# Performance work log

Measured on AMD Instinct MI355X. Metric: run time of the kernel, lower is better.

Reference implementation:

```python
import jax, jax.numpy as jnp
import numpy as np

HW = 24       # image_size // patch_size
HEAD = 16     # vision num_attention_heads
B, T, C, H = 8, 8, 1024, 4096


def _sincos_1d(d, pos):
    omega = np.arange(d // 2, dtype=np.float32) / (d / 2.0)
    omega = 1.0 / 10000 ** omega
    out = np.einsum('m,d->md', pos.reshape(-1).astype(np.float32), omega)
    return np.concatenate([np.sin(out), np.cos(out)], axis=1)


def _pos_embed_3d(embed_dim, grid_size, t_size):
    ds = embed_dim // 4 * 3
    dt = embed_dim // 4
    gh = np.arange(grid_size, dtype=np.float32)
    grid = np.stack(np.meshgrid(gh, gh), axis=0).reshape(2, -1)  # (w, h) order as in source
    spatial = np.concatenate([_sincos_1d(ds // 2, grid[0]), _sincos_1d(ds // 2, grid[1])], axis=1)  # [g*g, ds]
    temporal = _sincos_1d(dt, np.arange(t_size, dtype=np.float32))  # [t, dt]
    spatial = np.repeat(spatial[np.newaxis], t_size, axis=0)                 # [t, g*g, ds]
    temporal = np.repeat(temporal[:, np.newaxis], grid_size ** 2, axis=1)    # [t, g*g, dt]
    emb = np.concatenate([temporal, spatial], axis=-1)
    return emb.reshape(1, t_size * grid_size ** 2, embed_dim).astype(np.float32)


def setup_inputs() -> dict:
    key = jax.random.key(0)
    k1, k2, k3 = jax.random.split(key, 3)
    x = jax.random.normal(k1, (B, T * HW * HW, C), dtype=jnp.float32)
    W1 = jax.random.normal(k2, (C, H), dtype=jnp.float32) * 0.02
    b1 = jnp.zeros((H,), jnp.float32)
    W2 = jax.random.normal(k3, (H, H), dtype=jnp.float32) * 0.02
    b2 = jnp.zeros((H,), jnp.float32)
    pos_embed = jnp.asarray(_pos_embed_3d(C, HW, T))
    return {"x": x, "pos_embed": pos_embed, "W1": W1, "b1": b1, "W2": W2, "b2": b2,
            "local_num_frames": T}


def _merge(x, unm_idx, src_idx, dst_idx):
    # ToMe merge: gather unmatched src tokens, scatter-add matched src into dst.
    src, dst = x[:, ::2], x[:, 1::2]
    unm = jnp.take_along_axis(src, unm_idx[:, :, None], axis=1)   # [b, t1-r, c]
    sel = jnp.take_along_axis(src, src_idx[:, :, None], axis=1)   # [b, r, c]
    dst = jax.vmap(lambda d, i, s: d.at[i].add(s))(dst, dst_idx, sel)
    return jnp.concatenate([unm, dst], axis=1)


def _merge_tokens(x, target, head):
    b, p, c = x.shape
    # static merge schedule (same logic as torch merge_tokens)
    rs, tmp = [], p
    while tmp != target:
        if tmp - target <= tmp // 2:
            rs.append(tmp - target)
            break
        rs.append(tmp // 2)
        tmp -= tmp // 2
    dim = c // head
    size = jnp.ones((b, p, 1), x.dtype)
    for r in rs:
        bb, pp, _ = x.shape
        # metric/index computation is under no_grad in the original
        metric = jax.lax.stop_gradient(x).reshape(bb, pp, head, dim).mean(2)
        metric = metric / jnp.linalg.norm(metric, axis=-1, keepdims=True)
        a_m, b_m = metric[:, ::2], metric[:, 1::2]
        scores = jnp.einsum('bic,bjc->bij', a_m, b_m)  # [b, ta, tb]
        node_max = scores.max(-1)
        node_idx = scores.argmax(-1)
        edge_idx = jnp.argsort(-node_max, axis=-1)      # descending
        unm_idx, src_idx = edge_idx[:, r:], edge_idx[:, :r]
        dst_idx = jnp.take_along_axis(node_idx, src_idx, axis=1)
        # weighted-average merge (merge_wavg)
        x = _merge(x * size, unm_idx, src_idx, dst_idx)
        size = _merge(size, unm_idx, src_idx, dst_idx)
        x = x / size
    return x


def reference(x, pos_embed, W1, b1, W2, b2, local_num_frames):
    x = x + pos_embed.astype(x.dtype)
    x = _merge_tokens(x, local_num_frames * 16, HEAD)
    h = jax.nn.gelu(x @ W1 + b1, approximate=False)  # nn.GELU() is exact erf gelu
    return h @ W2 + b2
```

## Files before the change

### kernel.cpp

```cpp
#include <hip/hip_runtime.h>
#include <hip/hip_bf16.h>
#include <math.h>
#include <stdint.h>

typedef unsigned short u16;
typedef __attribute__((ext_vector_type(8))) short short8;
typedef __attribute__((ext_vector_type(4))) float floatx4;

#define NB 8
#define P0 4608
#define C0 1024
#define H0 4096

__global__ void detect_mode_kernel(const uint32_t* __restrict__ pe_words, int* __restrict__ mode) {
  *mode = (pe_words[64] != 0u) ? 1 : 0;
}

__device__ __forceinline__ float load_in(const void* p, size_t idx, int mode) {
  if (mode) return __bfloat162float(((const __hip_bfloat16*)p)[idx]);
  return ((const float*)p)[idx];
}

__device__ __forceinline__ float4 load4(const void* p, size_t idx, int mode) {
  float4 r;
  if (mode) {
    ushort4 u = *(const ushort4*)((const u16*)p + idx);
    r.x = __bfloat162float(*(__hip_bfloat16*)&u.x);
    r.y = __bfloat162float(*(__hip_bfloat16*)&u.y);
    r.z = __bfloat162float(*(__hip_bfloat16*)&u.z);
    r.w = __bfloat162float(*(__hip_bfloat16*)&u.w);
  } else {
    r = *(const float4*)((const float*)p + idx);
  }
  return r;
}

__device__ __forceinline__ void write_hilo(u16* __restrict__ m2, size_t tok, int lane, float v) {
  __hip_bfloat16 hi = __float2bfloat16(v);
  float hif = __bfloat162float(hi);
  __hip_bfloat16 lo = __float2bfloat16(v - hif);
  m2[tok * 128 + lane] = *(u16*)&hi;
  m2[tok * 128 + 64 + lane] = *(u16*)&lo;
}

__global__ void metric_in_kernel(const void* __restrict__ x, const void* __restrict__ pos,
                                 const int* __restrict__ mode, u16* __restrict__ m2) {
  int tok = blockIdx.x * 4 + (threadIdx.x >> 6);
  int lane = threadIdx.x & 63;
  if (tok >= NB * P0) return;
  int b = tok / P0, t = tok - b * P0;
  int md = *mode;
  size_t xbase = ((size_t)b * P0 + t) * C0 + lane;
  size_t pbase = (size_t)t * C0 + lane;
  float s = 0.f;
#pragma unroll
  for (int h = 0; h < 16; ++h)
    s += load_in(x, xbase + h * 64, md) + load_in(pos, pbase + h * 64, md);
  s *= (1.f / 16.f);
  float sq = s * s;
#pragma unroll
  for (int off = 1; off < 64; off <<= 1) sq += __shfl_xor(sq, off, 64);
  write_hilo(m2, (size_t)tok, lane, s / sqrtf(sq));
}

__global__ void metric_f32_kernel(const float* __restrict__ x, u16* __restrict__ m2, int p) {
  int tok = blockIdx.x * 4 + (threadIdx.x >> 6);
  int lane = threadIdx.x & 63;
  if (tok >= NB * p) return;
  const float* xr = x + (size_t)tok * C0 + lane;
  float s = 0.f;
#pragma unroll
  for (int h = 0; h < 16; ++h) s += xr[h * 64];
  s *= (1.f / 16.f);
  float sq = s * s;
#pragma unroll
  for (int off = 1; off < 64; off <<= 1) sq += __shfl_xor(sq, off, 64);
  write_hilo(m2, (size_t)tok, lane, s / sqrtf(sq));
}

__global__ __launch_bounds__(256) void score_mfma_kernel(const u16* __restrict__ M2,
                                                         int p, int p2, int jT2,
                                                         float* __restrict__ pm,
                                                         int* __restrict__ pi) {
  const int bi = blockIdx.x, ii = blockIdx.y, b = blockIdx.z;
  const int t = threadIdx.x, w = t >> 6, L = t & 63;
  const int wr = w >> 1, wc = w & 1;
  const int fr = L & 15, fo = (L >> 4) * 8;
  const u16* Mb = M2 + (size_t)b * p * 128;

  floatx4 acc[4][4];
#pragma unroll
  for (int mt = 0; mt < 4; ++mt)
#pragma unroll
    for (int nt = 0; nt < 4; ++nt) acc[mt][nt] = (floatx4){0.f, 0.f, 0.f, 0.f};

  const u16* arp[4];
  const u16* brp[4];
#pragma unroll
  for (int mt = 0; mt < 4; ++mt) {
    int i = ii * 128 + wr * 64 + mt * 16 + fr;
    int ta = 2 * i;
    if (ta > p - 2) ta = p - 2;
    arp[mt] = Mb + (size_t)ta * 128 + fo;
    int j = bi * 128 + wc * 64 + mt * 16 + fr;
    int tb = 2 * j + 1;
    if (tb > p - 1) tb = p - 1;
    brp[mt] = Mb + (size_t)tb * 128 + fo;
  }

#pragma unroll
  for (int ks = 0; ks < 2; ++ks) {
    short8 ah[4], al[4], bh[4], bl[4];
#pragma unroll
    for (int mt = 0; mt < 4; ++mt) {
      ah[mt] = *(const short8*)(arp[mt] + ks * 32);
      al[mt] = *(const short8*)(arp[mt] + ks * 32 + 64);
      bh[mt] = *(const short8*)(brp[mt] + ks * 32);
      bl[mt] = *(const short8*)(brp[mt] + ks * 32 + 64);
    }
#pragma unroll
    for (int mt = 0; mt < 4; ++mt)
#pragma unroll
      for (int nt = 0; nt < 4; ++nt) {
        acc[mt][nt] = __builtin_amdgcn_mfma_f32_16x16x32_bf16(ah[mt], bh[nt], acc[mt][nt], 0, 0, 0);
        acc[mt][nt] = __builtin_amdgcn_mfma_f32_16x16x32_bf16(ah[mt], bl[nt], acc[mt][nt], 0, 0, 0);
        acc[mt][nt] = __builtin_amdgcn_mfma_f32_16x16x32_bf16(al[mt], bh[nt], acc[mt][nt], 0, 0, 0);
        acc[mt][nt] = __builtin_amdgcn_mfma_f32_16x16x32_bf16(al[mt], bl[nt], acc[mt][nt], 0, 0, 0);
      }
  }

  const int gi4 = (L >> 4) * 4;
#pragma unroll
  for (int mt = 0; mt < 4; ++mt) {
#pragma unroll
    for (int reg = 0; reg < 4; ++reg) {
      int i = ii * 128 + wr * 64 + mt * 16 + gi4 + reg;
      float bm = -INFINITY;
      int bj = 0x7fffffff;
#pragma unroll
      for (int nt = 0; nt < 4; ++nt) {
        int j = bi * 128 + wc * 64 + nt * 16 + fr;
        float v = acc[mt][nt][reg];
        if (j < p2 && v > bm) { bm = v; bj = j; }
      }
#pragma unroll
      for (int mk = 1; mk < 16; mk <<= 1) {
        float om = __shfl_xor(bm, mk, 64);
        int oj = __shfl_xor(bj, mk, 64);
        if (om > bm || (om == bm && oj < bj)) { bm = om; bj = oj; }
      }
      if (fr == 0 && i < p2) {
        size_t o = ((size_t)b * 2304 + i) * jT2 + bi * 2 + wc;
        pm[o] = bm;
        pi[o] = bj;
      }
    }
  }
}

__global__ void argmax_combine_kernel(const float* __restrict__ pm, const int* __restrict__ pi,
                                      int p2, int jT, float* __restrict__ nmax,
                                      int* __restrict__ nidx, int* __restrict__ head,
                                      int* __restrict__ nxt) {
  int g = blockIdx.x * 256 + threadIdx.x;
  if (g >= NB * p2) return;
  int b = g / p2, i = g - b * p2;
  const float* r = pm + ((size_t)b * 2304 + i) * jT;
  const int* ri = pi + ((size_t)b * 2304 + i) * jT;
  float best = r[0];
  int bidx = ri[0];
  for (int k = 1; k < jT; ++k) {
    if (r[k] > best || (r[k] == best && ri[k] < bidx)) { best = r[k]; bidx = ri[k]; }
  }
  nmax[g] = best;
  nidx[g] = bidx;
  int d = bidx;
  if ((unsigned)d >= (unsigned)p2) d = 0;
  nxt[g] = atomicExch(&head[(size_t)b * p2 + d], i);
}

__global__ void init_heads_kernel(int* __restrict__ h, int n) {
  int g = blockIdx.x * 256 + threadIdx.x;
  if (g < n) h[g] = -1;
}

__global__ __launch_bounds__(256) void merge_gather_in(const void* __restrict__ x,
                                                       const void* __restrict__ pos,
                                                       const int* __restrict__ mode,
                                                       const int* __restrict__ head,
                                                       const int* __restrict__ nxt,
                                                       float* __restrict__ xo,
                                                       float* __restrict__ so, int p2) {
  int tj = blockIdx.x;
  int b = tj / p2, j = tj - b * p2;
  int c = threadIdx.x * 4;
  int md = *mode;
  __shared__ int sl[64];
  __shared__ int s_n, s_cur;
  size_t xb = ((size_t)b * P0 + 2 * j + 1) * C0 + c;
  size_t pb = (size_t)(2 * j + 1) * C0 + c;
  float4 xa = load4(x, xb, md), pa = load4(pos, pb, md);
  float4 acc = {xa.x + pa.x, xa.y + pa.y, xa.z + pa.z, xa.w + pa.w};
  float cnt = 1.f;
  if (threadIdx.x == 0) s_cur = head[tj];
  __syncthreads();
  int cur = s_cur;
  while (cur != -1) {
    if (threadIdx.x == 0) {
      int n = 0, cc = cur;
      while (cc != -1 && n < 64) {
        sl[n++] = cc;
        cc = nxt[(size_t)b * p2 + cc];
      }
      s_n = n;
      s_cur = cc;
    }
    __syncthreads();
    int n = s_n;
    cur = s_cur;
    for (int k = 0; k < n; ++k) {
      int i = sl[k];
      size_t exb = ((size_t)b * P0 + 2 * i) * C0 + c;
      size_t epb = (size_t)(2 * i) * C0 + c;
      float4 ea = load4(x, exb, md), ep = load4(pos, epb, md);
      acc.x += ea.x + ep.x;
      acc.y += ea.y + ep.y;
      acc.z += ea.z + ep.z;
      acc.w += ea.w + ep.w;
      cnt += 1.f;
    }
    __syncthreads();
  }
  float inv = 1.f / cnt;
  float4 o = {acc.x * inv, acc.y * inv, acc.z * inv, acc.w * inv};
  *(float4*)(xo + (size_t)tj * C0 + c) = o;
  if (threadIdx.x == 0) so[tj] = cnt;
}

__global__ __launch_bounds__(256) void merge_gather_f(const float* __restrict__ xi,
                                                      const float* __restrict__ si,
                                                      const int* __restrict__ head,
                                                      const int* __restrict__ nxt,
                                                      float* __restrict__ xo,
                                                      float* __restrict__ so, int p, int p2) {
  int tj = blockIdx.x;
  int b = tj / p2, j = tj - b * p2;
  int c = threadIdx.x * 4;
  __shared__ int sl[64];
  __shared__ int s_n, s_cur;
  float sz = si[(size_t)b * p + 2 * j + 1];
  float4 v = *(const float4*)(xi + ((size_t)b * p + 2 * j + 1) * C0 + c);
  float4 acc = {v.x * sz, v.y * sz, v.z * sz, v.w * sz};
  float ssum = sz;
  if (threadIdx.x == 0) s_cur = head[tj];
  __syncthreads();
  int cur = s_cur;
  while (cur != -1) {
    if (threadIdx.x == 0) {
      int n = 0, cc = cur;
      while (cc != -1 && n < 64) {
        sl[n++] = cc;
        cc = nxt[(size_t)b * p2 + cc];
      }
      s_n = n;
      s_cur = cc;
    }
    __syncthreads();
    int n = s_n;
    cur = s_cur;
    for (int k = 0; k < n; ++k) {
      int i = sl[k];
      float szi = si[(size_t)b * p + 2 * i];
      float4 e = *(const float4*)(xi + ((size_t)b * p + 2 * i) * C0 + c);
      acc.x += e.x * szi;
      acc.y += e.y * szi;
      acc.z += e.z * szi;
      acc.w += e.w * szi;
      ssum += szi;
    }
    __syncthreads();
  }
  float inv = 1.f / ssum;
  float4 o = {acc.x * inv, acc.y * inv, acc.z * inv, acc.w * inv};
  *(float4*)(xo + (size_t)tj * C0 + c) = o;
  if (threadIdx.x == 0) so[tj] = ssum;
}

__global__ void rank_kernel(const float* __restrict__ nmax, const int* __restrict__ nidx,
                            int* __restrict__ unm_map, int* __restrict__ src_ord,
                            int* __restrict__ src_dst) {
  int b = blockIdx.x;
  int i = threadIdx.x;
  __shared__ float v[72];
  __shared__ int nx[72];
  if (i < 72) { v[i] = nmax[b * 72 + i]; nx[i] = nidx[b * 72 + i]; }
  __syncthreads();
  if (i < 72) {
    float vi = v[i];
    int rank = 0;
    for (int k = 0; k < 72; ++k) {
      float vk = v[k];
      rank += (vk > vi) || (vk == vi && k < i);
    }
    if (rank < 16) {
      int d = nx[i];
      if ((unsigned)d >= 72u) d = 0;
      src_ord[b * 16 + rank] = i;
      src_dst[b * 16 + rank] = d;
    } else {
      unm_map[b * 56 + (rank - 16)] = i;
    }
  }
}

__global__ void final_init(const float* __restrict__ x5, const float* __restrict__ s5,
                           const int* __restrict__ unm_map, float* __restrict__ xf,
                           float* __restrict__ sf) {
  int bt = blockIdx.x;
  int b = bt >> 7, tk = bt & 127;
  int c = threadIdx.x * 4;
  float4 o;
  float szo;
  if (tk < 56) {
    int se = unm_map[b * 56 + tk];
    if ((unsigned)se >= 72u) se = 0;
    o = *(const float4*)(x5 + ((size_t)b * 144 + 2 * se) * C0 + c);
    szo = 1.f;
  } else {
    int j = tk - 56;
    float sz = s5[b * 144 + 2 * j + 1];
    float4 v = *(const float4*)(x5 + ((size_t)b * 144 + 2 * j + 1) * C0 + c);
    o.x = v.x * sz; o.y = v.y * sz; o.z = v.z * sz; o.w = v.w * sz;
    szo = sz;
  }
  *(float4*)(xf + (size_t)bt * C0 + c) = o;
  if (threadIdx.x == 0) sf[bt] = szo;
}

__global__ void final_scatter(const float* __restrict__ x5, const float* __restrict__ s5,
                              const int* __restrict__ src_ord, const int* __restrict__ src_dst,
                              float* __restrict__ xf, float* __restrict__ sf) {
  int bk = blockIdx.x;
  int b = bk >> 4, k = bk & 15;
  int c = threadIdx.x * 4;
  int st = src_ord[b * 16 + k], dst = src_dst[b * 16 + k];
  if ((unsigned)st >= 72u) st = 0;
  if ((unsigned)dst >= 72u) dst = 0;
  float sz = s5[b * 144 + 2 * st];
  float4 v = *(const float4*)(x5 + ((size_t)b * 144 + 2 * st) * C0 + c);
  float* out = xf + ((size_t)(b * 128 + 56 + dst)) * C0 + c;
  atomicAdd(out + 0, v.x * sz);
  atomicAdd(out + 1, v.y * sz);
  atomicAdd(out + 2, v.z * sz);
  atomicAdd(out + 3, v.w * sz);
  if (threadIdx.x == 0) atomicAdd(sf + b * 128 + 56 + dst, sz);
}

__global__ void final_div_cvt(const float* __restrict__ xf, const float* __restrict__ sf,
                              __hip_bfloat16* __restrict__ xb) {
  int bt = blockIdx.x;
  int c = threadIdx.x * 4;
  float sz = sf[bt];
  float4 v = *(const float4*)(xf + (size_t)bt * C0 + c);
  __hip_bfloat16* o = xb + (size_t)bt * C0 + c;
  o[0] = __float2bfloat16(v.x / sz);
  o[1] = __float2bfloat16(v.y / sz);
  o[2] = __float2bfloat16(v.z / sz);
  o[3] = __float2bfloat16(v.w / sz);
}

__global__ void transpose_in(const void* __restrict__ in, const int* __restrict__ mode,
                             u16* __restrict__ out, int K, int N) {
  __shared__ u16 tile[64][65];
  int n0 = blockIdx.x * 64, k0 = blockIdx.y * 64;
  int t = threadIdx.x;
  int md = *mode;
  int r = t >> 4, c4 = (t & 15) * 4;
#pragma unroll
  for (int pass = 0; pass < 4; ++pass) {
    int row = r + pass * 16;
#pragma unroll
    for (int e = 0; e < 4; ++e) {
      float v = load_in(in, (size_t)(k0 + row) * N + n0 + c4 + e, md);
      __hip_bfloat16 bv = __float2bfloat16(v);
      tile[row][c4 + e] = *(u16*)&bv;
    }
  }
  __syncthreads();
#pragma unroll
  for (int pass = 0; pass < 4; ++pass) {
    int row = r + pass * 16;
    ushort4 o;
    o.x = tile[c4][row]; o.y = tile[c4 + 1][row]; o.z = tile[c4 + 2][row]; o.w = tile[c4 + 3][row];
    *(ushort4*)(out + (size_t)(n0 + row) * K + k0 + c4) = o;
  }
}

__global__ __launch_bounds__(256) void gemm_bt(const u16* __restrict__ A,
                                               const u16* __restrict__ BT,
                                               const void* __restrict__ bias,
                                               const int* __restrict__ mode,
                                               void* __restrict__ C, int M, int N,
                                               int K, int act, int out_sel) {
  __shared__ __align__(16) u16 As[128 * 64];
  __shared__ __align__(16) u16 Bs[128 * 64];
  const int t = threadIdx.x, w = t >> 6, L = t & 63;
  const int m0 = blockIdx.y * 128, n0 = blockIdx.x * 128;
  const int wr = w >> 1, wc = w & 1;
  const int md = *mode;
  floatx4 acc[4][4];
#pragma unroll
  for (int a = 0; a < 4; ++a)
#pragma unroll
    for (int bb = 0; bb < 4; ++bb) acc[a][bb] = (floatx4){0.f, 0.f, 0.f, 0.f};
  const int fr = L & 15, fq = (L >> 4) * 8;
  const int srow = t >> 3, sc8 = (t & 7) * 8;
  for (int k0 = 0; k0 < K; k0 += 64) {
#pragma unroll
    for (int q = 0; q < 4; ++q) {
      int row = srow + q * 32;
      *(short8*)(As + row * 64 + sc8) =
          *(const short8*)(A + (size_t)(m0 + row) * K + k0 + sc8);
      *(short8*)(Bs + row * 64 + sc8) =
          *(const short8*)(BT + (size_t)(n0 + row) * K + k0 + sc8);
    }
    __syncthreads();
#pragma unroll
    for (int kh = 0; kh < 2; ++kh) {
      short8 af[4], bfr[4];
#pragma unroll
      for (int mt = 0; mt < 4; ++mt)
        af[mt] = *(const short8*)(As + (wr * 64 + mt * 16 + fr) * 64 + kh * 32 + fq);
#pragma unroll
      for (int nt = 0; nt < 4; ++nt)
        bfr[nt] = *(const short8*)(Bs + (wc * 64 + nt * 16 + fr) * 64 + kh * 32 + fq);
#pragma unroll
      for (int mt = 0; mt < 4; ++mt)
#pragma unroll
        for (int nt = 0; nt < 4; ++nt)
          acc[mt][nt] =
              __builtin_amdgcn_mfma_f32_16x16x32_bf16(af[mt], bfr[nt], acc[mt][nt], 0, 0, 0);
    }
    __syncthreads();
  }
#pragma unroll
  for (int mt = 0; mt < 4; ++mt)
#pragma unroll
    for (int nt = 0; nt < 4; ++nt) {
      int n = n0 + wc * 64 + nt * 16 + fr;
      float bz = load_in(bias, n, md);
#pragma unroll
      for (int rr = 0; rr < 4; ++rr) {
        int m = m0 + wr * 64 + mt * 16 + (L >> 4) * 4 + rr;
        float v = acc[mt][nt][rr] + bz;
        if (act) v = 0.5f * v * (1.f + erff(v * 0.70710678118654752f));
        size_t idx = (size_t)m * N + n;
        if (out_sel == 0 || md) {
          __hip_bfloat16 bv = __float2bfloat16(v);
          ((u16*)C)[idx] = *(u16*)&bv;
        } else {
          ((float*)C)[idx] = v;
        }
      }
    }
}

extern "C" void kernel_launch(void* const* d_in, const int* in_sizes, int n_in, void* d_out,
                              int out_size, void* d_ws, size_t ws_size, hipStream_t stream) {
  const void* x = d_in[0];
  const void* pe = d_in[1];
  const void* W1 = d_in[2];
  const void* b1 = d_in[3];
  const void* W2 = d_in[4];
  const void* b2 = d_in[5];

  char* base = (char*)d_ws;
  size_t off = 0;
  auto alloc = [&](size_t bytes) -> void* {
    void* p = base + off;
    off += (bytes + 255) & ~(size_t)255;
    return p;
  };
  int* mode = (int*)alloc(256);
  u16* m2 = (u16*)alloc((size_t)NB * 4608 * 128 * 2);
  float* pm = (float*)alloc((size_t)NB * 2304 * 36 * 4);
  int* pi = (int*)alloc((size_t)NB * 2304 * 36 * 4);
  float* nmax = (float*)alloc((size_t)NB * 2304 * 4);
  int* nidx = (int*)alloc((size_t)NB * 2304 * 4);
  float* bufA = (float*)alloc((size_t)NB * 2304 * C0 * 4);
  float* bufB = (float*)alloc((size_t)NB * 1152 * C0 * 4);
  float* s1 = (float*)alloc((size_t)NB * 2304 * 4);
  float* s2 = (float*)alloc((size_t)NB * 1152 * 4);
  float* s3 = (float*)alloc((size_t)NB * 576 * 4);
  float* s4 = (float*)alloc((size_t)NB * 288 * 4);
  float* s5 = (float*)alloc((size_t)NB * 144 * 4);
  float* sf = (float*)alloc((size_t)NB * 128 * 4);
  int* unm_map = (int*)alloc((size_t)NB * 56 * 4);
  int* src_ord = (int*)alloc((size_t)NB * 16 * 4);
  int* src_dst = (int*)alloc((size_t)NB * 16 * 4);
  u16* xfb = (u16*)alloc((size_t)NB * 128 * C0 * 2);
  u16* hbuf = (u16*)alloc((size_t)1024 * H0 * 2);
  u16* w1t = (u16*)alloc((size_t)H0 * C0 * 2);
  u16* w2t = (u16*)alloc((size_t)H0 * H0 * 2);
  int* heads = (int*)alloc((size_t)NB * 4536 * 4);
  int* nxt = (int*)alloc((size_t)NB * 2304 * 4);
  if (off > ws_size) return;

  int* h_it[6];
  h_it[0] = heads;
  h_it[1] = h_it[0] + NB * 2304;
  h_it[2] = h_it[1] + NB * 1152;
  h_it[3] = h_it[2] + NB * 576;
  h_it[4] = h_it[3] + NB * 288;
  h_it[5] = h_it[4] + NB * 144;

  float* x1 = bufA;
  float* x2 = bufB;
  float* x3 = bufA;
  float* x4 = bufB;
  float* x5 = bufA;
  float* xf = bufB;

  detect_mode_kernel<<<1, 1, 0, stream>>>((const uint32_t*)pe, mode);
  init_heads_kernel<<<(NB * 4536 + 255) / 256, 256, 0, stream>>>(heads, NB * 4536);

  transpose_in<<<dim3(4096 / 64, 1024 / 64), 256, 0, stream>>>(W1, mode, w1t, 1024, 4096);
  transpose_in<<<dim3(4096 / 64, 4096 / 64), 256, 0, stream>>>(W2, mode, w2t, 4096, 4096);

  metric_in_kernel<<<NB * P0 / 4, 256, 0, stream>>>(x, pe, mode, m2);
  score_mfma_kernel<<<dim3(18, 18, NB), 256, 0, stream>>>(m2, 4608, 2304, 36, pm, pi);
  argmax_combine_kernel<<<(NB * 2304 + 255) / 256, 256, 0, stream>>>(pm, pi, 2304, 36, nmax,
                                                                     nidx, h_it[0], nxt);
  merge_gather_in<<<NB * 2304, 256, 0, stream>>>(x, pe, mode, h_it[0], nxt, x1, s1, 2304);

  float* xs_in[4] = {x1, x2, x3, x4};
  float* ss_in[4] = {s1, s2, s3, s4};
  float* xs_out[4] = {x2, x3, x4, x5};
  float* ss_out[4] = {s2, s3, s4, s5};
  int ps[5] = {2304, 1152, 576, 288, 144};
  for (int it = 0; it < 4; ++it) {
    int p = ps[it], p2 = ps[it + 1];
    int iT = (p2 + 127) / 128, jT = (p2 + 127) / 128;
    metric_f32_kernel<<<NB * p / 4, 256, 0, stream>>>(xs_in[it], m2, p);
    score_mfma_kernel<<<dim3(jT, iT, NB), 256, 0, stream>>>(m2, p, p2, 2 * jT, pm, pi);
    argmax_combine_kernel<<<(NB * p2 + 255) / 256, 256, 0, stream>>>(pm, pi, p2, 2 * jT, nmax,
                                                                     nidx, h_it[it + 1], nxt);
    merge_gather_f<<<NB * p2, 256, 0, stream>>>(xs_in[it], ss_in[it], h_it[it + 1], nxt,
                                                xs_out[it], ss_out[it], p, p2);
  }

  metric_f32_kernel<<<NB * 144 / 4, 256, 0, stream>>>(x5, m2, 144);
  score_mfma_kernel<<<dim3(1, 1, NB), 256, 0, stream>>>(m2, 144, 72, 2, pm, pi);
  argmax_combine_kernel<<<(NB * 72 + 255) / 256, 256, 0, stream>>>(pm, pi, 72, 2, nmax, nidx,
                                                                   h_it[5], nxt);
  rank_kernel<<<NB, 128, 0, stream>>>(nmax, nidx, unm_map, src_ord, src_dst);
  final_init<<<NB * 128, 256, 0, stream>>>(x5, s5, unm_map, xf, sf);
  final_scatter<<<NB * 16, 256, 0, stream>>>(x5, s5, src_ord, src_dst, xf, sf);
  final_div_cvt<<<NB * 128, 256, 0, stream>>>(xf, sf, (__hip_bfloat16*)xfb);

  gemm_bt<<<dim3(4096 / 128, 1024 / 128), 256, 0, stream>>>(xfb, w1t, b1, mode, hbuf, 1024, 4096,
                                                            1024, 1, 0);
  gemm_bt<<<dim3(4096 / 128, 1024 / 128), 256, 0, stream>>>(hbuf, w2t, b2, mode, d_out, 1024,
                                                            4096, 4096, 0, 1);
}
```

Before: 834.7 us.

## Double-buffer GEMM tiles via direct global-to-LDS loads and shrink M tile

The bf16 GEMM now stages A and B tiles straight into LDS with global_load_lds and double buffers them, so the next K-slice loads while MFMAs run on the current one. The M tile drops from 128 to 64, doubling the block count to 512 so the MI355X CUs stay busier on these 1024-row GEMMs. In exchange each block does fewer MFMAs per byte loaded, and B tiles are fetched twice as often across blocks.

```diff
diff --git a/kernel.cpp b/kernel.cpp
--- a/kernel.cpp
+++ b/kernel.cpp
@@ -396,62 +396,80 @@
   }
 }
 
+#define GL2LDS(gp, lp)                                                                   \
+  __builtin_amdgcn_global_load_lds((const __attribute__((address_space(1))) uint32_t*)(gp), \
+                                   (__attribute__((address_space(3))) uint32_t*)(lp), 16, 0, 0)
+
 __global__ __launch_bounds__(256) void gemm_bt(const u16* __restrict__ A,
                                                const u16* __restrict__ BT,
                                                const void* __restrict__ bias,
                                                const int* __restrict__ mode,
                                                void* __restrict__ C, int M, int N,
                                                int K, int act, int out_sel) {
-  __shared__ __align__(16) u16 As[128 * 64];
-  __shared__ __align__(16) u16 Bs[128 * 64];
+  __shared__ __align__(16) u16 As[2 * 64 * 64];
+  __shared__ __align__(16) u16 Bs[2 * 128 * 64];
   const int t = threadIdx.x, w = t >> 6, L = t & 63;
-  const int m0 = blockIdx.y * 128, n0 = blockIdx.x * 128;
+  const int m0 = blockIdx.y * 64, n0 = blockIdx.x * 128;
   const int wr = w >> 1, wc = w & 1;
   const int md = *mode;
-  floatx4 acc[4][4];
-#pragma unroll
-  for (int a = 0; a < 4; ++a)
+  const int fr = L & 15, fq = (L >> 4) * 8;
+  const int trow = t >> 3, tc8 = (t & 7) * 8;
+  floatx4 acc[2][4];
+#pragma unroll
+  for (int a = 0; a < 2; ++a)
 #pragma unroll
     for (int bb = 0; bb < 4; ++bb) acc[a][bb] = (floatx4){0.f, 0.f, 0.f, 0.f};
-  const int fr = L & 15, fq = (L >> 4) * 8;
-  const int srow = t >> 3, sc8 = (t & 7) * 8;
+
+  auto stage = [&](int buf, int kk) {
+#pragma unroll
+    for (int q = 0; q < 2; ++q)
+      GL2LDS(A + (size_t)(m0 + q * 32 + trow) * K + kk + tc8,
+             As + buf * 4096 + q * 2048 + t * 8);
+#pragma unroll
+    for (int q = 0; q < 4; ++q)
+      GL2LDS(BT + (size_t)(n0 + q * 32 + trow) * K + kk + tc8,
+             Bs + buf * 8192 + q * 2048 + t * 8);
+  };
+
+  stage(0, 0);
+  asm volatile("s_waitcnt vmcnt(0)" ::: "memory");
+  __builtin_amdgcn_s_barrier();
+  int cur = 0;
   for (int k0 = 0; k0 < K; k0 += 64) {
-#pragma unroll
-    for (int q = 0; q < 4; ++q) {
-      int row = srow + q * 32;
-      *(short8*)(As + row * 64 + sc8) =
-          *(const short8*)(A + (size_t)(m0 + row) * K + k0 + sc8);
-      *(short8*)(Bs + row * 64 + sc8) =
-          *(const short8*)(BT + (size_t)(n0 + row) * K + k0 + sc8);
-    }
-    __syncthreads();
+    int kn = k0 + 64;
+    if (kn < K) stage(cur ^ 1, kn);
+    const u16* Ab = As + cur * 4096;
+    const u16* Bb = Bs + cur * 8192;
 #pragma unroll
     for (int kh = 0; kh < 2; ++kh) {
-      short8 af[4], bfr[4];
-#pragma unroll
-      for (int mt = 0; mt < 4; ++mt)
-        af[mt] = *(const short8*)(As + (wr * 64 + mt * 16 + fr) * 64 + kh * 32 + fq);
+      short8 af[2], bfr[4];
+#pragma unroll
+      for (int mt = 0; mt < 2; ++mt)
+        af[mt] = *(const short8*)(Ab + (wr * 32 + mt * 16 + fr) * 64 + kh * 32 + fq);
 #pragma unroll
       for (int nt = 0; nt < 4; ++nt)
-        bfr[nt] = *(const short8*)(Bs + (wc * 64 + nt * 16 + fr) * 64 + kh * 32 + fq);
-#pragma unroll
-      for (int mt = 0; mt < 4; ++mt)
+        bfr[nt] = *(const short8*)(Bb + (wc * 64 + nt * 16 + fr) * 64 + kh * 32 + fq);
+#pragma unroll
+      for (int mt = 0; mt < 2; ++mt)
 #pragma unroll
         for (int nt = 0; nt < 4; ++nt)
           acc[mt][nt] =
               __builtin_amdgcn_mfma_f32_16x16x32_bf16(af[mt], bfr[nt], acc[mt][nt], 0, 0, 0);
     }
-    __syncthreads();
-  }
-#pragma unroll
-  for (int mt = 0; mt < 4; ++mt)
+    asm volatile("s_waitcnt vmcnt(0)" ::: "memory");
+    __builtin_amdgcn_s_barrier();
+    cur ^= 1;
+  }
+  const int gi4 = (L >> 4) * 4;
+#pragma unroll
+  for (int mt = 0; mt < 2; ++mt)
 #pragma unroll
     for (int nt = 0; nt < 4; ++nt) {
       int n = n0 + wc * 64 + nt * 16 + fr;
       float bz = load_in(bias, n, md);
 #pragma unroll
       for (int rr = 0; rr < 4; ++rr) {
-        int m = m0 + wr * 64 + mt * 16 + (L >> 4) * 4 + rr;
+        int m = m0 + wr * 32 + mt * 16 + gi4 + rr;
         float v = acc[mt][nt][rr] + bz;
         if (act) v = 0.5f * v * (1.f + erff(v * 0.70710678118654752f));
         size_t idx = (size_t)m * N + n;
@@ -558,8 +576,8 @@
   final_scatter<<<NB * 16, 256, 0, stream>>>(x5, s5, src_ord, src_dst, xf, sf);
   final_div_cvt<<<NB * 128, 256, 0, stream>>>(xf, sf, (__hip_bfloat16*)xfb);
 
-  gemm_bt<<<dim3(4096 / 128, 1024 / 128), 256, 0, stream>>>(xfb, w1t, b1, mode, hbuf, 1024, 4096,
-                                                            1024, 1, 0);
-  gemm_bt<<<dim3(4096 / 128, 1024 / 128), 256, 0, stream>>>(hbuf, w2t, b2, mode, d_out, 1024,
-                                                            4096, 4096, 0, 1);
-}
+  gemm_bt<<<dim3(4096 / 128, 1024 / 64), 256, 0, stream>>>(xfb, w1t, b1, mode, hbuf, 1024, 4096,
+                                                           1024, 1, 0);
+  gemm_bt<<<dim3(4096 / 128, 1024 / 64), 256, 0, stream>>>(hbuf, w2t, b2, mode, d_out, 1024,
+                                                           4096, 4096, 0, 1);
+}
```

Result: faster. 794.8 us (-4.8%).
